# Kernel tuning notes

Measured on AMD Instinct MI355X. Metric: run time of the kernel, lower is better.

## Reference

```python
import jax, jax.numpy as jnp
import numpy as np

BATCH, SEQ = 2, 2048
HID = 2048          # hidden_size
INTER = 4096        # intermediate_size
STATE = 16          # ssm_state_size
RANK = 128          # time_step_rank
K = 4               # conv_kernel


def setup_inputs() -> dict:
    key = jax.random.key(0)
    ks = jax.random.split(key, 8)
    s = 0.02
    return {
        "hidden_states": jax.random.normal(ks[0], (BATCH, SEQ, HID), jnp.float32),
        "in_proj_w": jax.random.normal(ks[1], (2 * INTER, HID), jnp.float32) * s,
        "conv_w": jax.random.normal(ks[2], (INTER, 1, K), jnp.float32) * s,   # depthwise (O, I/g=1, K)
        "conv_b": jnp.zeros((INTER,), jnp.float32),
        "x_proj_w": jax.random.normal(ks[3], (RANK + 2 * STATE, INTER), jnp.float32) * s,
        "dt_proj_w": jax.random.normal(ks[4], (INTER, RANK), jnp.float32) * s,
        "dt_proj_b": jax.random.normal(ks[5], (INTER,), jnp.float32) * s,
        "A_log": jnp.log(jnp.broadcast_to(jnp.arange(1, STATE + 1, dtype=jnp.float32), (INTER, STATE))),
        "D": jnp.ones((INTER,), jnp.float32),
        "out_proj_w": jax.random.normal(ks[6], (HID, INTER), jnp.float32) * s,
    }


def reference(hidden_states, in_proj_w, conv_w, conv_b, x_proj_w,
              dt_proj_w, dt_proj_b, A_log, D, out_proj_w):
    B, L, _ = hidden_states.shape
    # in_proj -> (B, L, 2*INTER), split into u (SSM input) and gate
    proj = jnp.einsum('blh,ph->blp', hidden_states, in_proj_w)
    u, gate = jnp.split(proj, 2, axis=-1)                       # (B, L, INTER) each
    # depthwise causal conv1d on channel-major layout (B, INTER, L)
    uc = jnp.swapaxes(u, 1, 2)
    conv = jax.lax.conv_general_dilated(
        uc, conv_w, window_strides=(1,), padding=[(K - 1, 0)],
        dimension_numbers=('NCH', 'OIH', 'NCH'), feature_group_count=INTER)
    u = jax.nn.silu(conv + conv_b[None, :, None])               # (B, INTER, L)
    # x_proj: dt-rank + B + C, computed in fp32 like the original
    ssm_p = jnp.einsum('bdl,pd->blp', u, x_proj_w).astype(jnp.float32)
    dt_r, Bm, Cm = jnp.split(ssm_p, [RANK, RANK + STATE], axis=-1)  # (B,L,RANK),(B,L,N),(B,L,N)
    dt = jax.nn.softplus(jnp.einsum('blr,dr->bld', dt_r, dt_proj_w) + dt_proj_b)  # (B, L, INTER)
    A = -jnp.exp(A_log)                                         # (INTER, STATE)

    def step(state, xs):
        dt_t, B_t, C_t, u_t = xs                                # (B,D),(B,N),(B,N),(B,D)
        dA = jnp.exp(dt_t[:, :, None] * A[None])                # (B, D, N)
        state = dA * state + (dt_t * u_t)[:, :, None] * B_t[:, None, :]
        y = jnp.einsum('bdn,bn->bd', state, C_t)
        return state, y

    xs = (jnp.swapaxes(dt, 0, 1),        # (L, B, D)
          jnp.swapaxes(Bm, 0, 1),        # (L, B, N)
          jnp.swapaxes(Cm, 0, 1),        # (L, B, N)
          jnp.moveaxis(u, 2, 0))         # (L, B, D)
    init = jnp.zeros((B, INTER, STATE), jnp.float32)
    _, ys = jax.lax.scan(step, init, xs)                        # (L, B, D)

    y = jnp.moveaxis(ys, 0, 1) + jnp.swapaxes(u, 1, 2) * D[None, None, :]  # skip connection
    y = y * jax.nn.silu(gate)
    return jnp.einsum('bld,hd->blh', y, out_proj_w)             # (B, L, HID)
```

## Files before the change

### kernel.cpp

```cpp
#include <hip/hip_runtime.h>

typedef unsigned int u32;
typedef unsigned short u16;
typedef float f32x4 __attribute__((ext_vector_type(4)));
typedef u16 us4 __attribute__((ext_vector_type(4)));
typedef u16 us8 __attribute__((ext_vector_type(8)));
typedef __bf16 bf16x8 __attribute__((ext_vector_type(8)));

__device__ __forceinline__ u16 f2bf(float f) {
  u32 u = __builtin_bit_cast(u32, f);
  u += 0x7fffu + ((u >> 16) & 1u);
  return (u16)(u >> 16);
}
__device__ __forceinline__ float bf2f(u16 h) {
  u32 u = ((u32)h) << 16;
  return __builtin_bit_cast(float, u);
}
__device__ __forceinline__ void async16(const void* g, void* l) {
  __builtin_amdgcn_global_load_lds((const __attribute__((address_space(1))) void*)g,
                                   (__attribute__((address_space(3))) void*)l, 16, 0, 0);
}

template <int ACT, bool SPLITK = false>
__global__ __launch_bounds__(256) void gemm_bt(const u16* __restrict__ A,
                                               const u16* __restrict__ B,
                                               void* __restrict__ Cv,
                                               const float* __restrict__ bias,
                                               int K, int ldc) {
  __shared__ __align__(16) u16 As[128 * 64];
  __shared__ __align__(16) u16 Bs[128 * 64];
  const int tid = threadIdx.x;
  const int lane = tid & 63;
  const int wave = tid >> 6;
  const int lm = lane & 15;
  const int quad = lane >> 4;
  const int wm = (wave >> 1) << 6;
  const int wn = (wave & 1) << 6;
  const long rowBase = (long)blockIdx.y << 7;
  const long colBase = (long)blockIdx.x << 7;

  int kStart = 0, kEnd = K;
  if constexpr (SPLITK) {
    int kn = K / gridDim.z;
    kStart = blockIdx.z * kn;
    kEnd = kStart + kn;
  }

  const int rr = tid >> 3;
  const int qg = (tid & 7) ^ (rr & 7);
  const u16* Ag = A + (rowBase + rr) * (long)K + qg * 8;
  const u16* Bg = B + (colBase + rr) * (long)K + qg * 8;
  u16* Al = As + tid * 8;
  u16* Bl = Bs + tid * 8;

  f32x4 acc[4][4] = {};
  const int l7 = lm & 7;

  for (int k0 = kStart; k0 < kEnd; k0 += 64) {
#pragma unroll
    for (int c = 0; c < 4; ++c) {
      async16(Ag + 32L * c * K + k0, Al + 2048 * c);
      async16(Bg + 32L * c * K + k0, Bl + 2048 * c);
    }
    __syncthreads();
#pragma unroll
    for (int h = 0; h < 2; ++h) {
      const int xa = ((h * 4 + quad) ^ l7) * 8;
      us8 af[4], bfr[4];
#pragma unroll
      for (int i = 0; i < 4; ++i)
        af[i] = *(const us8*)(As + (wm + i * 16 + lm) * 64 + xa);
#pragma unroll
      for (int i = 0; i < 4; ++i)
        bfr[i] = *(const us8*)(Bs + (wn + i * 16 + lm) * 64 + xa);
#pragma unroll
      for (int i = 0; i < 4; ++i)
#pragma unroll
        for (int j = 0; j < 4; ++j)
          acc[i][j] = __builtin_amdgcn_mfma_f32_16x16x32_bf16(
              __builtin_bit_cast(bf16x8, af[i]), __builtin_bit_cast(bf16x8, bfr[j]),
              acc[i][j], 0, 0, 0);
    }
    __syncthreads();
  }

  float* Cf = (float*)Cv;
  if constexpr (SPLITK)
    Cf += (size_t)blockIdx.z * ((size_t)gridDim.y * 128 * ldc);

#pragma unroll
  for (int i = 0; i < 4; ++i)
#pragma unroll
    for (int j = 0; j < 4; ++j)
#pragma unroll
      for (int r = 0; r < 4; ++r) {
        long row = rowBase + wm + i * 16 + quad * 4 + r;
        long col = colBase + wn + j * 16 + lm;
        float v = acc[i][j][r];
        if constexpr (ACT == 0) {
          Cf[row * ldc + col] = v;
        } else if constexpr (ACT == 1) {
          ((u16*)Cv)[row * ldc + col] = f2bf(v);
        } else if constexpr (ACT == 2) {
          float s = v / (1.f + __expf(-v));
          ((u16*)Cv)[row * ldc + col] = f2bf(s);
        } else if constexpr (ACT == 3) {
          v += bias[col];
          float sp = (v > 20.f) ? v : log1pf(__expf(v));
          Cf[row * ldc + col] = sp;
        } else {
          if (colBase < 4096) {
            ((u16*)Cv)[row * 4096 + col] = f2bf(v);
          } else {
            float s = v / (1.f + __expf(-v));
            ((u16*)(size_t)bias)[row * 4096 + (col - 4096)] = f2bf(s);
          }
        }
      }
}

__global__ __launch_bounds__(256) void cvt_bf16(const float* __restrict__ in,
                                                u16* __restrict__ out, int n4) {
  int i = blockIdx.x * 256 + threadIdx.x;
  if (i >= n4) return;
  f32x4 v = ((const f32x4*)in)[i];
  us4 o;
  o[0] = f2bf(v[0]); o[1] = f2bf(v[1]); o[2] = f2bf(v[2]); o[3] = f2bf(v[3]);
  ((us4*)out)[i] = o;
}

__global__ __launch_bounds__(256) void cvt_xw(const float* __restrict__ in,
                                              u16* __restrict__ out) {
  int i = blockIdx.x * 256 + threadIdx.x;
  int row = (i << 2) >> 12;
  us4 o;
  if (row < 160) {
    f32x4 v = ((const f32x4*)in)[i];
    o[0] = f2bf(v[0]); o[1] = f2bf(v[1]); o[2] = f2bf(v[2]); o[3] = f2bf(v[3]);
  } else {
    o[0] = 0; o[1] = 0; o[2] = 0; o[3] = 0;
  }
  ((us4*)out)[i] = o;
}

__global__ __launch_bounds__(256) void xp_reduce(const float* __restrict__ part,
                                                 float* __restrict__ smp,
                                                 u16* __restrict__ dtrb) {
  int i = blockIdx.x * 256 + threadIdx.x;
  const f32x4* p = (const f32x4*)part;
  f32x4 v = p[i];
  v += p[i + 262144];
  v += p[i + 524288];
  v += p[i + 786432];
  ((f32x4*)smp)[i] = v;
  int e = i << 2;
  int c = e & 255;
  if (c < 128) {
    int t = e >> 8;
    us4 o;
    o[0] = f2bf(v[0]); o[1] = f2bf(v[1]); o[2] = f2bf(v[2]); o[3] = f2bf(v[3]);
    *(us4*)(dtrb + t * 128 + c) = o;
  }
}

__global__ __launch_bounds__(256) void conv_silu(const u16* __restrict__ U,
                                                 const float* __restrict__ cw,
                                                 const float* __restrict__ cb,
                                                 u16* __restrict__ out) {
  int i = blockIdx.x * 256 + threadIdx.x;
  int t = i >> 10;
  int d4 = (i & 1023) << 2;
  int l = t & 2047;
  float w[4][4];
#pragma unroll
  for (int j = 0; j < 4; ++j) {
    f32x4 wv = *(const f32x4*)(cw + (d4 + j) * 4);
    w[j][0] = wv[0]; w[j][1] = wv[1]; w[j][2] = wv[2]; w[j][3] = wv[3];
  }
  float r[4] = {cb[d4], cb[d4 + 1], cb[d4 + 2], cb[d4 + 3]};
#pragma unroll
  for (int k = 0; k < 4; ++k) {
    int ll = l - 3 + k;
    if (ll >= 0) {
      us4 xv = *(const us4*)(U + (size_t)(t - 3 + k) * 4096 + d4);
      r[0] += w[0][k] * bf2f(xv[0]);
      r[1] += w[1][k] * bf2f(xv[1]);
      r[2] += w[2][k] * bf2f(xv[2]);
      r[3] += w[3][k] * bf2f(xv[3]);
    }
  }
  us4 o;
#pragma unroll
  for (int j = 0; j < 4; ++j) {
    float v = r[j];
    float s = v / (1.f + __expf(-v));
    o[j] = f2bf(s);
  }
  *(us4*)(out + (size_t)t * 4096 + d4) = o;
}

__global__ __launch_bounds__(256) void scan_part(
    const float* __restrict__ dt, const u16* __restrict__ ub,
    const float* __restrict__ ssmp, const float* __restrict__ Alog,
    float* __restrict__ Pout, float* __restrict__ Sout) {
  const int tid = threadIdx.x;
  const int chunk = blockIdx.x, dgrp = blockIdx.y, b = blockIdx.z;
  const int d = (dgrp << 8) + tid;
  float A[16];
#pragma unroll
  for (int q = 0; q < 4; ++q) {
    f32x4 v = *(const f32x4*)(Alog + d * 16 + q * 4);
    A[q * 4 + 0] = -__expf(v[0]);
    A[q * 4 + 1] = -__expf(v[1]);
    A[q * 4 + 2] = -__expf(v[2]);
    A[q * 4 + 3] = -__expf(v[3]);
  }
  bool fastl = true;
#pragma unroll
  for (int n = 1; n < 16; ++n)
    fastl = fastl && (fabsf(A[n] - (n + 1) * A[0]) <= 1e-4f * (float)(n + 1));
  const bool fast = (__ballot(fastl) == ~0ull);

  const int base = b * 2048 + chunk * 128;
  const float* dtp = dt + (size_t)base * 4096 + d;
  const u16* up = ub + (size_t)base * 4096 + d;
  const float* Bp = ssmp + (size_t)base * 256 + 128;

  float s[16] = {};
  float dtsum = 0.f;
  float cdt[8], cu[8], ndt[8] = {}, nu[8] = {};
#pragma unroll
  for (int j = 0; j < 8; ++j) {
    cdt[j] = dtp[j * 4096];
    cu[j] = bf2f(up[j * 4096]);
  }
  for (int l0 = 0; l0 < 128; l0 += 8) {
    if (l0 + 8 < 128) {
      int o = (l0 + 8) * 4096;
#pragma unroll
      for (int j = 0; j < 8; ++j) {
        ndt[j] = dtp[o + j * 4096];
        nu[j] = bf2f(up[o + j * 4096]);
      }
    }
    if (fast) {
#pragma unroll
      for (int j = 0; j < 8; ++j) {
        float e1 = __expf(cdt[j] * A[0]);
        float x = cdt[j] * cu[j];
        const float* Bl = Bp + (l0 + j) * 256;
        f32x4 B0 = *(const f32x4*)(Bl);
        f32x4 B1 = *(const f32x4*)(Bl + 4);
        f32x4 B2 = *(const f32x4*)(Bl + 8);
        f32x4 B3 = *(const f32x4*)(Bl + 12);
        float p = 1.f;
#pragma unroll
        for (int n = 0; n < 16; ++n) {
          p *= e1;
          float Bn = (n < 4) ? B0[n & 3] : (n < 8) ? B1[n & 3] : (n < 12) ? B2[n & 3] : B3[n & 3];
          s[n] = fmaf(p, s[n], x * Bn);
        }
        dtsum += cdt[j];
      }
    } else {
#pragma unroll
      for (int j = 0; j < 8; ++j) {
        float x = cdt[j] * cu[j];
        const float* Bl = Bp + (l0 + j) * 256;
        f32x4 B0 = *(const f32x4*)(Bl);
        f32x4 B1 = *(const f32x4*)(Bl + 4);
        f32x4 B2 = *(const f32x4*)(Bl + 8);
        f32x4 B3 = *(const f32x4*)(Bl + 12);
#pragma unroll
        for (int n = 0; n < 16; ++n) {
          float e = __expf(cdt[j] * A[n]);
          float Bn = (n < 4) ? B0[n & 3] : (n < 8) ? B1[n & 3] : (n < 12) ? B2[n & 3] : B3[n & 3];
          s[n] = fmaf(e, s[n], x * Bn);
        }
        dtsum += cdt[j];
      }
    }
#pragma unroll
    for (int j = 0; j < 8; ++j) { cdt[j] = ndt[j]; cu[j] = nu[j]; }
  }
  size_t o = (((size_t)(b * 4096 + d)) * 16 + chunk) * 16;
#pragma unroll
  for (int n = 0; n < 16; ++n) {
    Pout[o + n] = __expf(dtsum * A[n]);
    Sout[o + n] = s[n];
  }
}

__global__ __launch_bounds__(256) void scan_y(
    const float* __restrict__ dt, const u16* __restrict__ ub,
    const float* __restrict__ ssmp, const u16* __restrict__ gs,
    const float* __restrict__ Alog, const float* __restrict__ Dv,
    const float* __restrict__ Pin, const float* __restrict__ Sin,
    u16* __restrict__ yb) {
  const int tid = threadIdx.x;
  const int chunk = blockIdx.x, dgrp = blockIdx.y, b = blockIdx.z;
  const int d = (dgrp << 8) + tid;
  float A[16];
#pragma unroll
  for (int q = 0; q < 4; ++q) {
    f32x4 v = *(const f32x4*)(Alog + d * 16 + q * 4);
    A[q * 4 + 0] = -__expf(v[0]);
    A[q * 4 + 1] = -__expf(v[1]);
    A[q * 4 + 2] = -__expf(v[2]);
    A[q * 4 + 3] = -__expf(v[3]);
  }
  bool fastl = true;
#pragma unroll
  for (int n = 1; n < 16; ++n)
    fastl = fastl && (fabsf(A[n] - (n + 1) * A[0]) <= 1e-4f * (float)(n + 1));
  const bool fast = (__ballot(fastl) == ~0ull);
  const float Dd = Dv[d];

  const int base = b * 2048 + chunk * 128;
  const float* dtp = dt + (size_t)base * 4096 + d;
  const u16* up = ub + (size_t)base * 4096 + d;
  const u16* gp = gs + (size_t)base * 4096 + d;
  const float* Bp = ssmp + (size_t)base * 256 + 128;
  u16* yo = yb + (size_t)base * 4096 + d;

  float s[16] = {};
  {
    size_t po = ((size_t)(b * 4096 + d)) * 256;
    for (int k = 0; k < chunk; ++k) {
      const float* Pk = Pin + po + k * 16;
      const float* Sk = Sin + po + k * 16;
#pragma unroll
      for (int q = 0; q < 4; ++q) {
        f32x4 P = *(const f32x4*)(Pk + 4 * q);
        f32x4 S = *(const f32x4*)(Sk + 4 * q);
        s[4 * q + 0] = fmaf(P[0], s[4 * q + 0], S[0]);
        s[4 * q + 1] = fmaf(P[1], s[4 * q + 1], S[1]);
        s[4 * q + 2] = fmaf(P[2], s[4 * q + 2], S[2]);
        s[4 * q + 3] = fmaf(P[3], s[4 * q + 3], S[3]);
      }
    }
  }

  float cdt[8], cu[8], cg[8], ndt[8] = {}, nu[8] = {}, ng[8] = {};
#pragma unroll
  for (int j = 0; j < 8; ++j) {
    cdt[j] = dtp[j * 4096];
    cu[j] = bf2f(up[j * 4096]);
    cg[j] = bf2f(gp[j * 4096]);
  }
  for (int l0 = 0; l0 < 128; l0 += 8) {
    if (l0 + 8 < 128) {
      int o = (l0 + 8) * 4096;
#pragma unroll
      for (int j = 0; j < 8; ++j) {
        ndt[j] = dtp[o + j * 4096];
        nu[j] = bf2f(up[o + j * 4096]);
        ng[j] = bf2f(gp[o + j * 4096]);
      }
    }
    if (fast) {
#pragma unroll
      for (int j = 0; j < 8; ++j) {
        float e1 = __expf(cdt[j] * A[0]);
        float x = cdt[j] * cu[j];
        const float* Bl = Bp + (l0 + j) * 256;
        f32x4 B0 = *(const f32x4*)(Bl);
        f32x4 B1 = *(const f32x4*)(Bl + 4);
        f32x4 B2 = *(const f32x4*)(Bl + 8);
        f32x4 B3 = *(const f32x4*)(Bl + 12);
        f32x4 C0 = *(const f32x4*)(Bl + 16);
        f32x4 C1 = *(const f32x4*)(Bl + 20);
        f32x4 C2 = *(const f32x4*)(Bl + 24);
        f32x4 C3 = *(const f32x4*)(Bl + 28);
        float p = 1.f;
        float y0 = 0.f, y1 = 0.f, y2 = 0.f, y3 = 0.f;
#pragma unroll
        for (int n = 0; n < 16; ++n) {
          p *= e1;
          float Bn = (n < 4) ? B0[n & 3] : (n < 8) ? B1[n & 3] : (n < 12) ? B2[n & 3] : B3[n & 3];
          float Cn = (n < 4) ? C0[n & 3] : (n < 8) ? C1[n & 3] : (n < 12) ? C2[n & 3] : C3[n & 3];
          s[n] = fmaf(p, s[n], x * Bn);
          if (n < 4) y0 = fmaf(s[n], Cn, y0);
          else if (n < 8) y1 = fmaf(s[n], Cn, y1);
          else if (n < 12) y2 = fmaf(s[n], Cn, y2);
          else y3 = fmaf(s[n], Cn, y3);
        }
        float y = (y0 + y1) + (y2 + y3);
        yo[(l0 + j) * 4096] = f2bf((y + cu[j] * Dd) * cg[j]);
      }
    } else {
#pragma unroll
      for (int j = 0; j < 8; ++j) {
        float x = cdt[j] * cu[j];
        const float* Bl = Bp + (l0 + j) * 256;
        f32x4 B0 = *(const f32x4*)(Bl);
        f32x4 B1 = *(const f32x4*)(Bl + 4);
        f32x4 B2 = *(const f32x4*)(Bl + 8);
        f32x4 B3 = *(const f32x4*)(Bl + 12);
        f32x4 C0 = *(const f32x4*)(Bl + 16);
        f32x4 C1 = *(const f32x4*)(Bl + 20);
        f32x4 C2 = *(const f32x4*)(Bl + 24);
        f32x4 C3 = *(const f32x4*)(Bl + 28);
        float y0 = 0.f, y1 = 0.f, y2 = 0.f, y3 = 0.f;
#pragma unroll
        for (int n = 0; n < 16; ++n) {
          float e = __expf(cdt[j] * A[n]);
          float Bn = (n < 4) ? B0[n & 3] : (n < 8) ? B1[n & 3] : (n < 12) ? B2[n & 3] : B3[n & 3];
          float Cn = (n < 4) ? C0[n & 3] : (n < 8) ? C1[n & 3] : (n < 12) ? C2[n & 3] : C3[n & 3];
          s[n] = fmaf(e, s[n], x * Bn);
          if (n < 4) y0 = fmaf(s[n], Cn, y0);
          else if (n < 8) y1 = fmaf(s[n], Cn, y1);
          else if (n < 12) y2 = fmaf(s[n], Cn, y2);
          else y3 = fmaf(s[n], Cn, y3);
        }
        float y = (y0 + y1) + (y2 + y3);
        yo[(l0 + j) * 4096] = f2bf((y + cu[j] * Dd) * cg[j]);
      }
    }
#pragma unroll
    for (int j = 0; j < 8; ++j) { cdt[j] = ndt[j]; cu[j] = nu[j]; cg[j] = ng[j]; }
  }
}

extern "C" void kernel_launch(void* const* d_in, const int* in_sizes, int n_in,
                              void* d_out, int out_size, void* d_ws,
                              size_t ws_size, hipStream_t stream) {
  (void)in_sizes; (void)n_in; (void)out_size; (void)ws_size;
  const float* hs = (const float*)d_in[0];
  const float* wIn = (const float*)d_in[1];
  const float* cw = (const float*)d_in[2];
  const float* cb = (const float*)d_in[3];
  const float* wX = (const float*)d_in[4];
  const float* wDt = (const float*)d_in[5];
  const float* bDt = (const float*)d_in[6];
  const float* Alog = (const float*)d_in[7];
  const float* Dv = (const float*)d_in[8];
  const float* wOut = (const float*)d_in[9];

  const size_t MB = 1ull << 20;
  char* w = (char*)d_ws;
  u16* Xb = (u16*)(w + 0 * MB);
  u16* Winb = (u16*)(w + 16 * MB);
  u16* Pu = (u16*)(w + 48 * MB);
  float* DtF = (float*)(w + 0 * MB);
  u16* Yb = (u16*)(w + 64 * MB);
  u16* Ub = (u16*)(w + 96 * MB);
  u16* Wxb = (u16*)(w + 128 * MB);
  float* Smp = (float*)(w + 130 * MB);
  u16* Dtrb = (u16*)(w + 134 * MB);
  u16* Wdtb = (u16*)(w + 135 * MB);
  u16* Wob = (u16*)(w + 136 * MB);
  float* Pchk = (float*)(w + 152 * MB);
  float* Schk = (float*)(w + 160 * MB);
  float* Xpart = (float*)(w + 168 * MB);
  u16* Pg = (u16*)d_out;

  cvt_bf16<<<8192, 256, 0, stream>>>(hs, Xb, 2097152);
  cvt_bf16<<<16384, 256, 0, stream>>>(wIn, Winb, 4194304);
  cvt_xw<<<1024, 256, 0, stream>>>(wX, Wxb);
  cvt_bf16<<<512, 256, 0, stream>>>(wDt, Wdtb, 131072);
  cvt_bf16<<<8192, 256, 0, stream>>>(wOut, Wob, 2097152);

  gemm_bt<5><<<dim3(64, 32), 256, 0, stream>>>(Xb, Winb, Pu, (const float*)Pg, 2048, 4096);
  conv_silu<<<16384, 256, 0, stream>>>(Pu, cw, cb, Ub);
  gemm_bt<0, true><<<dim3(2, 32, 4), 256, 0, stream>>>(Ub, Wxb, Xpart, nullptr, 4096, 256);
  xp_reduce<<<1024, 256, 0, stream>>>(Xpart, Smp, Dtrb);
  gemm_bt<3><<<dim3(32, 32), 256, 0, stream>>>(Dtrb, Wdtb, DtF, bDt, 128, 4096);
  scan_part<<<dim3(16, 16, 2), 256, 0, stream>>>(DtF, Ub, Smp, Alog, Pchk, Schk);
  scan_y<<<dim3(16, 16, 2), 256, 0, stream>>>(DtF, Ub, Smp, Pg, Alog, Dv, Pchk, Schk, Yb);
  gemm_bt<0><<<dim3(16, 32), 256, 0, stream>>>(Yb, Wob, (float*)d_out, nullptr, 4096, 2048);
}
```

Measured before the change: 687.8 us.

## Store dt in bf16, merge conversion kernels, transpose chunk-state layout

The dt projection now writes softplus output as bf16 instead of fp32, which halves the dt traffic read by both scan kernels. The five fp32-to-bf16 conversion launches are merged into one kernel to cut launch overhead. The per-chunk P/S state buffers are relaid out with d as the fastest index, so the scans' stores and the prefix loads are coalesced across threads. Holding dt in bf16 adds rounding error to the exponent used in the recurrence.

```diff
diff --git a/kernel.cpp b/kernel.cpp
--- a/kernel.cpp
+++ b/kernel.cpp
@@ -108,6 +108,10 @@
           v += bias[col];
           float sp = (v > 20.f) ? v : log1pf(__expf(v));
           Cf[row * ldc + col] = sp;
+        } else if constexpr (ACT == 4) {
+          v += bias[col];
+          float sp = (v > 20.f) ? v : log1pf(__expf(v));
+          ((u16*)Cv)[row * ldc + col] = f2bf(sp);
         } else {
           if (colBase < 4096) {
             ((u16*)Cv)[row * 4096 + col] = f2bf(v);
@@ -119,28 +123,37 @@
       }
 }
 
-__global__ __launch_bounds__(256) void cvt_bf16(const float* __restrict__ in,
-                                                u16* __restrict__ out, int n4) {
-  int i = blockIdx.x * 256 + threadIdx.x;
-  if (i >= n4) return;
+__device__ __forceinline__ void cvt4(const float* __restrict__ in,
+                                     u16* __restrict__ out, int i) {
   f32x4 v = ((const f32x4*)in)[i];
   us4 o;
   o[0] = f2bf(v[0]); o[1] = f2bf(v[1]); o[2] = f2bf(v[2]); o[3] = f2bf(v[3]);
   ((us4*)out)[i] = o;
 }
-
-__global__ __launch_bounds__(256) void cvt_xw(const float* __restrict__ in,
-                                              u16* __restrict__ out) {
+__global__ __launch_bounds__(256) void cvt_all(
+    const float* __restrict__ hs, const float* __restrict__ wIn,
+    const float* __restrict__ wOut, const float* __restrict__ wDt,
+    const float* __restrict__ wX, u16* __restrict__ Xb, u16* __restrict__ Winb,
+    u16* __restrict__ Wob, u16* __restrict__ Wdtb, u16* __restrict__ Wxb) {
   int i = blockIdx.x * 256 + threadIdx.x;
+  if (i < 2097152) { cvt4(hs, Xb, i); return; }
+  i -= 2097152;
+  if (i < 4194304) { cvt4(wIn, Winb, i); return; }
+  i -= 4194304;
+  if (i < 2097152) { cvt4(wOut, Wob, i); return; }
+  i -= 2097152;
+  if (i < 131072) { cvt4(wDt, Wdtb, i); return; }
+  i -= 131072;
+  if (i >= 262144) return;
   int row = (i << 2) >> 12;
   us4 o;
   if (row < 160) {
-    f32x4 v = ((const f32x4*)in)[i];
+    f32x4 v = ((const f32x4*)wX)[i];
     o[0] = f2bf(v[0]); o[1] = f2bf(v[1]); o[2] = f2bf(v[2]); o[3] = f2bf(v[3]);
   } else {
     o[0] = 0; o[1] = 0; o[2] = 0; o[3] = 0;
   }
-  ((us4*)out)[i] = o;
+  ((us4*)Wxb)[i] = o;
 }
 
 __global__ __launch_bounds__(256) void xp_reduce(const float* __restrict__ part,
@@ -200,7 +213,7 @@
 }
 
 __global__ __launch_bounds__(256) void scan_part(
-    const float* __restrict__ dt, const u16* __restrict__ ub,
+    const u16* __restrict__ dt, const u16* __restrict__ ub,
     const float* __restrict__ ssmp, const float* __restrict__ Alog,
     float* __restrict__ Pout, float* __restrict__ Sout) {
   const int tid = threadIdx.x;
@@ -222,7 +235,7 @@
   const bool fast = (__ballot(fastl) == ~0ull);
 
   const int base = b * 2048 + chunk * 128;
-  const float* dtp = dt + (size_t)base * 4096 + d;
+  const u16* dtp = dt + (size_t)base * 4096 + d;
   const u16* up = ub + (size_t)base * 4096 + d;
   const float* Bp = ssmp + (size_t)base * 256 + 128;
 
@@ -231,7 +244,7 @@
   float cdt[8], cu[8], ndt[8] = {}, nu[8] = {};
 #pragma unroll
   for (int j = 0; j < 8; ++j) {
-    cdt[j] = dtp[j * 4096];
+    cdt[j] = bf2f(dtp[j * 4096]);
     cu[j] = bf2f(up[j * 4096]);
   }
   for (int l0 = 0; l0 < 128; l0 += 8) {
@@ -239,7 +252,7 @@
       int o = (l0 + 8) * 4096;
 #pragma unroll
       for (int j = 0; j < 8; ++j) {
-        ndt[j] = dtp[o + j * 4096];
+        ndt[j] = bf2f(dtp[o + j * 4096]);
         nu[j] = bf2f(up[o + j * 4096]);
       }
     }
@@ -283,16 +296,16 @@
 #pragma unroll
     for (int j = 0; j < 8; ++j) { cdt[j] = ndt[j]; cu[j] = nu[j]; }
   }
-  size_t o = (((size_t)(b * 4096 + d)) * 16 + chunk) * 16;
+  size_t o = ((size_t)(b * 16 + chunk) * 16) * 4096 + d;
 #pragma unroll
   for (int n = 0; n < 16; ++n) {
-    Pout[o + n] = __expf(dtsum * A[n]);
-    Sout[o + n] = s[n];
+    Pout[o + (size_t)n * 4096] = __expf(dtsum * A[n]);
+    Sout[o + (size_t)n * 4096] = s[n];
   }
 }
 
 __global__ __launch_bounds__(256) void scan_y(
-    const float* __restrict__ dt, const u16* __restrict__ ub,
+    const u16* __restrict__ dt, const u16* __restrict__ ub,
     const float* __restrict__ ssmp, const u16* __restrict__ gs,
     const float* __restrict__ Alog, const float* __restrict__ Dv,
     const float* __restrict__ Pin, const float* __restrict__ Sin,
@@ -317,7 +330,7 @@
   const float Dd = Dv[d];
 
   const int base = b * 2048 + chunk * 128;
-  const float* dtp = dt + (size_t)base * 4096 + d;
+  const u16* dtp = dt + (size_t)base * 4096 + d;
   const u16* up = ub + (size_t)base * 4096 + d;
   const u16* gp = gs + (size_t)base * 4096 + d;
   const float* Bp = ssmp + (size_t)base * 256 + 128;
@@ -325,18 +338,13 @@
 
   float s[16] = {};
   {
-    size_t po = ((size_t)(b * 4096 + d)) * 256;
     for (int k = 0; k < chunk; ++k) {
-      const float* Pk = Pin + po + k * 16;
-      const float* Sk = Sin + po + k * 16;
-#pragma unroll
-      for (int q = 0; q < 4; ++q) {
-        f32x4 P = *(const f32x4*)(Pk + 4 * q);
-        f32x4 S = *(const f32x4*)(Sk + 4 * q);
-        s[4 * q + 0] = fmaf(P[0], s[4 * q + 0], S[0]);
-        s[4 * q + 1] = fmaf(P[1], s[4 * q + 1], S[1]);
-        s[4 * q + 2] = fmaf(P[2], s[4 * q + 2], S[2]);
-        s[4 * q + 3] = fmaf(P[3], s[4 * q + 3], S[3]);
+      size_t o = ((size_t)(b * 16 + k) * 16) * 4096 + d;
+#pragma unroll
+      for (int n = 0; n < 16; ++n) {
+        float P = Pin[o + (size_t)n * 4096];
+        float S = Sin[o + (size_t)n * 4096];
+        s[n] = fmaf(P, s[n], S);
       }
     }
   }
@@ -344,7 +352,7 @@
   float cdt[8], cu[8], cg[8], ndt[8] = {}, nu[8] = {}, ng[8] = {};
 #pragma unroll
   for (int j = 0; j < 8; ++j) {
-    cdt[j] = dtp[j * 4096];
+    cdt[j] = bf2f(dtp[j * 4096]);
     cu[j] = bf2f(up[j * 4096]);
     cg[j] = bf2f(gp[j * 4096]);
   }
@@ -353,7 +361,7 @@
       int o = (l0 + 8) * 4096;
 #pragma unroll
       for (int j = 0; j < 8; ++j) {
-        ndt[j] = dtp[o + j * 4096];
+        ndt[j] = bf2f(dtp[o + j * 4096]);
         nu[j] = bf2f(up[o + j * 4096]);
         ng[j] = bf2f(gp[o + j * 4096]);
       }
@@ -442,7 +450,7 @@
   u16* Xb = (u16*)(w + 0 * MB);
   u16* Winb = (u16*)(w + 16 * MB);
   u16* Pu = (u16*)(w + 48 * MB);
-  float* DtF = (float*)(w + 0 * MB);
+  u16* Dtb = (u16*)(w + 0 * MB);
   u16* Yb = (u16*)(w + 64 * MB);
   u16* Ub = (u16*)(w + 96 * MB);
   u16* Wxb = (u16*)(w + 128 * MB);
@@ -455,18 +463,13 @@
   float* Xpart = (float*)(w + 168 * MB);
   u16* Pg = (u16*)d_out;
 
-  cvt_bf16<<<8192, 256, 0, stream>>>(hs, Xb, 2097152);
-  cvt_bf16<<<16384, 256, 0, stream>>>(wIn, Winb, 4194304);
-  cvt_xw<<<1024, 256, 0, stream>>>(wX, Wxb);
-  cvt_bf16<<<512, 256, 0, stream>>>(wDt, Wdtb, 131072);
-  cvt_bf16<<<8192, 256, 0, stream>>>(wOut, Wob, 2097152);
-
+  cvt_all<<<34304, 256, 0, stream>>>(hs, wIn, wOut, wDt, wX, Xb, Winb, Wob, Wdtb, Wxb);
   gemm_bt<5><<<dim3(64, 32), 256, 0, stream>>>(Xb, Winb, Pu, (const float*)Pg, 2048, 4096);
   conv_silu<<<16384, 256, 0, stream>>>(Pu, cw, cb, Ub);
   gemm_bt<0, true><<<dim3(2, 32, 4), 256, 0, stream>>>(Ub, Wxb, Xpart, nullptr, 4096, 256);
   xp_reduce<<<1024, 256, 0, stream>>>(Xpart, Smp, Dtrb);
-  gemm_bt<3><<<dim3(32, 32), 256, 0, stream>>>(Dtrb, Wdtb, DtF, bDt, 128, 4096);
-  scan_part<<<dim3(16, 16, 2), 256, 0, stream>>>(DtF, Ub, Smp, Alog, Pchk, Schk);
-  scan_y<<<dim3(16, 16, 2), 256, 0, stream>>>(DtF, Ub, Smp, Pg, Alog, Dv, Pchk, Schk, Yb);
+  gemm_bt<4><<<dim3(32, 32), 256, 0, stream>>>(Dtrb, Wdtb, Dtb, bDt, 128, 4096);
+  scan_part<<<dim3(16, 16, 2), 256, 0, stream>>>(Dtb, Ub, Smp, Alog, Pchk, Schk);
+  scan_y<<<dim3(16, 16, 2), 256, 0, stream>>>(Dtb, Ub, Smp, Pg, Alog, Dv, Pchk, Schk, Yb);
   gemm_bt<0><<<dim3(16, 32), 256, 0, stream>>>(Yb, Wob, (float*)d_out, nullptr, 4096, 2048);
 }
```

After: 667.1 us. 3.0% less time.
